# Performance work log

Measured on AMD Instinct MI355X. Metric: run time of the kernel, lower is better.

Reference implementation:

```python
import jax, jax.numpy as jnp
import numpy as np

B, S, QD, KVD, H = 8, 1024, 1024, 1024, 8
NEG_SLOPE = 0.01


def _lin(t, w, b):
    # torch nn.Linear: y = x @ W^T + b, W is (out, in)
    return t @ w.T + b


def _heads(t, n_head):
    b, s, e = t.shape
    return t.reshape(b, s, n_head, e // n_head).transpose(0, 2, 1, 3)  # (B,H,S,D)


def _merge(t):
    b, h, s, d = t.shape
    return t.transpose(0, 2, 1, 3).reshape(b, s, h * d)


def setup_inputs() -> dict:
    key = jax.random.key(0)
    ks = iter(jax.random.split(key, 64))

    def W(shape):
        return (jax.random.normal(next(ks), shape, jnp.float32) * 0.02)

    inp = {
        'x': jax.random.normal(next(ks), (B, S, QD), jnp.float32),
        'y': jax.random.normal(next(ks), (B, S, KVD), jnp.float32),
        # cross-attention projections
        'ca_q_w': W((QD, QD)), 'ca_q_b': W((QD,)),
        'ca_qv_w': W((QD, QD)), 'ca_qv_b': W((QD,)),
        'ca_k_w': W((QD, KVD)), 'ca_k_b': W((QD,)),
        'ca_kv_w': W((QD, KVD)), 'ca_kv_b': W((QD,)),
        'ca_o_w': W((QD, QD)), 'ca_o_b': W((QD,)),
        # LayerNorm over [seq_len, q_dim]
        'ln_w': jnp.ones((S, QD), jnp.float32),
        'ln_b': jnp.zeros((S, QD), jnp.float32),
        # 3-layer FeedForward
        'ff1_w': W((QD, QD)), 'ff1_b': W((QD,)),
        'ff2_w': W((QD, QD)), 'ff2_b': W((QD,)),
        'ff3_w': W((QD, QD)), 'ff3_b': W((QD,)),
        # self-attention 1
        'sa1_q_w': W((QD, QD)), 'sa1_q_b': W((QD,)),
        'sa1_k_w': W((QD, QD)), 'sa1_k_b': W((QD,)),
        'sa1_v_w': W((QD, QD)), 'sa1_v_b': W((QD,)),
        'sa1_o_w': W((QD, QD)), 'sa1_o_b': W((QD,)),
        # self-attention 2
        'sa2_q_w': W((QD, QD)), 'sa2_q_b': W((QD,)),
        'sa2_k_w': W((QD, QD)), 'sa2_k_b': W((QD,)),
        'sa2_v_w': W((QD, QD)), 'sa2_v_b': W((QD,)),
        'sa2_o_w': W((QD, QD)), 'sa2_o_b': W((QD,)),
    }
    return inp


def _self_attn(t, qw, qb, kw, kb, vw, vb, ow, ob):
    q = _heads(_lin(t, qw, qb), H)
    k = _heads(_lin(t, kw, kb), H)
    v = _heads(_lin(t, vw, vb), H)
    scale = 1.0 / jnp.sqrt(jnp.asarray(q.shape[-1], q.dtype))
    a = jax.nn.softmax(jnp.einsum('bhsd,bhtd->bhst', q, k) * scale, axis=-1)
    return _lin(_merge(jnp.einsum('bhst,bhtd->bhsd', a, v)), ow, ob)


def reference(x, y, ca_q_w, ca_q_b, ca_qv_w, ca_qv_b, ca_k_w, ca_k_b, ca_kv_w, ca_kv_b, ca_o_w, ca_o_b, ln_w, ln_b, ff1_w, ff1_b, ff2_w, ff2_b, ff3_w, ff3_b, sa1_q_w, sa1_q_b, sa1_k_w, sa1_k_b, sa1_v_w, sa1_v_b, sa1_o_w, sa1_o_b, sa2_q_w, sa2_q_b, sa2_k_w, sa2_k_b, sa2_v_w, sa2_v_b, sa2_o_w, sa2_o_b):
    # --- FlowFace cross-attention (no 1/sqrt(d) scaling, +QV term) ---
    q = _heads(_lin(x, ca_q_w, ca_q_b), H)
    qv = _heads(_lin(x, ca_qv_w, ca_qv_b), H)
    k = _heads(_lin(y, ca_k_w, ca_k_b), H)
    kv = _heads(_lin(y, ca_kv_w, ca_kv_b), H)
    attn = jax.nn.softmax(jnp.einsum('bhsd,bhtd->bhst', q, k), axis=-1)
    ca = _lin(_merge(jnp.einsum('bhst,bhtd->bhsd', attn, kv) + qv), ca_o_w, ca_o_b)
    h1 = x + ca
    # --- LayerNorm over last two dims [seq_len, q_dim] ---
    mu = h1.mean(axis=(-2, -1), keepdims=True)
    var = h1.var(axis=(-2, -1), keepdims=True)
    hn = (h1 - mu) / jnp.sqrt(var + 1e-5) * ln_w + ln_b
    # --- 3-layer FeedForward with leaky_relu + residual ---
    lr = lambda t: jax.nn.leaky_relu(t, NEG_SLOPE)
    f = lr(_lin(lr(_lin(lr(_lin(hn, ff1_w, ff1_b)), ff2_w, ff2_b)), ff3_w, ff3_b))
    h2 = hn + f
    # --- two self-attention layers ---
    h3 = _self_attn(h2, sa1_q_w, sa1_q_b, sa1_k_w, sa1_k_b, sa1_v_w, sa1_v_b, sa1_o_w, sa1_o_b)
    out = _self_attn(h3, sa2_q_w, sa2_q_b, sa2_k_w, sa2_k_b, sa2_v_w, sa2_v_b, sa2_o_w, sa2_o_b)
    return out
```

## Files before the change

kernel.cpp:

```cpp
#include <hip/hip_runtime.h>
#include <cstdint>
#include <cstddef>

#define DI __device__ __forceinline__

typedef __bf16 bf16x8 __attribute__((ext_vector_type(8)));
typedef float  f32x4  __attribute__((ext_vector_type(4)));

constexpr int kE = 1024;
constexpr int kM = 8192;
constexpr float kSlope = 0.01f;

DI float bf2f(ushort u) { union { uint32_t i; float f; } v; v.i = ((uint32_t)u) << 16; return v.f; }
DI ushort f2bf(float f) {
    union { float f; uint32_t i; } v; v.f = f;
    return (ushort)((v.i + 0x7FFFu + ((v.i >> 16) & 1u)) >> 16);
}
DI bf16x8 ld8f(const float* p) {
    const float4 f0 = *(const float4*)p;
    const float4 f1 = *(const float4*)(p + 4);
    union { bf16x8 v; ushort u[8]; } o;
    o.u[0] = f2bf(f0.x); o.u[1] = f2bf(f0.y); o.u[2] = f2bf(f0.z); o.u[3] = f2bf(f0.w);
    o.u[4] = f2bf(f1.x); o.u[5] = f2bf(f1.y); o.u[6] = f2bf(f1.z); o.u[7] = f2bf(f1.w);
    return o.v;
}
template<typename T> DI float ldf(const T* p);
template<> DI float ldf<ushort>(const ushort* p) { return bf2f(*p); }
template<> DI float ldf<float>(const float* p) { return *p; }

DI void gload16(const void* g, void* lds) {
    __builtin_amdgcn_global_load_lds((const __attribute__((address_space(1))) void*)g,
                                     (__attribute__((address_space(3))) void*)lds, 16, 0, 0);
}

DI int swz7(int r) { return ((r ^ (r >> 3)) & 7) << 4; }

struct PtrTab { const float* w[16]; const float* b[16]; const float* x; const float* y; };

__global__ __launch_bounds__(256)
void cvt_pack(PtrTab t, ushort* __restrict__ WB, ushort* __restrict__ Xb,
              ushort* __restrict__ Yb, float* __restrict__ BP)
{
    const int blk = blockIdx.x, tid = threadIdx.x;
    if (blk < 16384) {
        const float* src; ushort* dst; size_t idx;
        if (blk < 8192)       { const int w = blk >> 9; idx = (size_t)(blk & 511) * 2048 + tid * 8; src = t.w[w]; dst = WB + (size_t)w * 1048576; }
        else if (blk < 12288) { idx = (size_t)(blk - 8192) * 2048 + tid * 8;  src = t.x; dst = Xb; }
        else                  { idx = (size_t)(blk - 12288) * 2048 + tid * 8; src = t.y; dst = Yb; }
        *(bf16x8*)(dst + idx) = ld8f(src + idx);
    } else {
        const size_t i = (size_t)(blk - 16384) * 2048 + tid * 8;
        const int w = (int)(i >> 10), off = (int)(i & 1023);
        *(float4*)(BP + i)     = *(const float4*)(t.b[w] + off);
        *(float4*)(BP + i + 4) = *(const float4*)(t.b[w] + off + 4);
    }
}

template<int ACT, int RESID, typename TR, typename TO>
__global__ __launch_bounds__(256)
void gemm_bf16(const ushort* __restrict__ A, const ushort* __restrict__ W,
               const float* __restrict__ bias, const TR* __restrict__ resb,
               TO* __restrict__ out, int N)
{
    __shared__ __align__(16) char sm[2][16384];
    constexpr int K = 1024;
    const int tid = threadIdx.x, l = tid & 63, wid = tid >> 6;
    const int wm = wid >> 1, wn = wid & 1;

    const int cpx = gridDim.x >> 3;
    const int sb = (blockIdx.x & 7) * cpx + (blockIdx.x >> 3);
    const int nbn = N >> 7;
    const int bm = sb / nbn, bn = sb - bm * nbn;
    const size_t row0 = (size_t)bm << 7, col0 = (size_t)bn << 7;

    const int o0 = (wid * 2) * 1024 + (l << 4), o1 = o0 + 1024;
    const int r0s = o0 >> 6, c0s = ((o0 >> 4) & 3) ^ ((r0s >> 1) & 3);
    const int r1s = o1 >> 6, c1s = ((o1 >> 4) & 3) ^ ((r1s >> 1) & 3);
    const ushort* gA0 = A + (row0 + r0s) * K + c0s * 8;
    const ushort* gA1 = A + (row0 + r1s) * K + c1s * 8;
    const ushort* gW0 = W + (col0 + r0s) * K + c0s * 8;
    const ushort* gW1 = W + (col0 + r1s) * K + c1s * 8;
    const int d0 = (wid * 2) * 1024, d1 = d0 + 1024;

    f32x4 acc[4][4] = {};

    {
        gload16(gA0, sm[0] + d0); gload16(gA1, sm[0] + d1);
        gload16(gW0, sm[0] + 8192 + d0); gload16(gW1, sm[0] + 8192 + d1);
    }
    __syncthreads();

    for (int kt = 0; kt < 32; ++kt) {
        const int cur = kt & 1;
        if (kt + 1 < 32) {
            const int ko = (kt + 1) << 5;
            char* nb = sm[cur ^ 1];
            gload16(gA0 + ko, nb + d0); gload16(gA1 + ko, nb + d1);
            gload16(gW0 + ko, nb + 8192 + d0); gload16(gW1 + ko, nb + 8192 + d1);
        }
        const char* At = sm[cur];
        const char* Wt = sm[cur] + 8192;
        bf16x8 af[4], bfr[4];
        #pragma unroll
        for (int mi = 0; mi < 4; ++mi) {
            const int r = (wm << 6) + (mi << 4) + (l & 15);
            af[mi] = *(const bf16x8*)(At + r * 64 + ((((l >> 4) ^ ((r >> 1) & 3))) << 4));
        }
        #pragma unroll
        for (int ni = 0; ni < 4; ++ni) {
            const int r = (wn << 6) + (ni << 4) + (l & 15);
            bfr[ni] = *(const bf16x8*)(Wt + r * 64 + ((((l >> 4) ^ ((r >> 1) & 3))) << 4));
        }
        #pragma unroll
        for (int mi = 0; mi < 4; ++mi)
            #pragma unroll
            for (int ni = 0; ni < 4; ++ni)
                acc[mi][ni] = __builtin_amdgcn_mfma_f32_16x16x32_bf16(af[mi], bfr[ni], acc[mi][ni], 0, 0, 0);
        __syncthreads();
    }

    const int cr = (l >> 4) << 2, cc = l & 15;
    #pragma unroll
    for (int mi = 0; mi < 4; ++mi) {
        #pragma unroll
        for (int ni = 0; ni < 4; ++ni) {
            const size_t gr = row0 + (wm << 6) + (mi << 4) + cr;
            const size_t gc = col0 + (wn << 6) + (ni << 4) + cc;
            const float bv = bias[gc];
            #pragma unroll
            for (int r = 0; r < 4; ++r) {
                float v = acc[mi][ni][r] + bv;
                if (ACT) v = v > 0.f ? v : v * kSlope;
                const size_t off = (gr + r) * (size_t)N + gc;
                if (RESID) v += ldf(resb + off);
                if constexpr (sizeof(TO) == 4) out[off] = v;
                else                           out[off] = f2bf(v);
            }
        }
    }
}

template<int ADD_QV>
__global__ __launch_bounds__(256)
void attn_fwd(const ushort* __restrict__ Q, const ushort* __restrict__ K,
              const ushort* __restrict__ V, const ushort* __restrict__ QV,
              ushort* __restrict__ O, int ld, float scale)
{
    __shared__ __align__(16) char Kt[64 * 256];
    __shared__ __align__(16) char Vt[128 * 128];
    __shared__ __align__(16) char Pl[4][2048];

    const int tid = threadIdx.x;
    const int l = tid & 63, w = tid >> 6;

    const int cpx = gridDim.x >> 3;
    const int sb = (blockIdx.x & 7) * cpx + (blockIdx.x >> 3);
    const int qt = sb & 15;
    const int bh = sb >> 4;
    const int h = bh & 7, b = bh >> 3;

    const size_t bi = ((size_t)b << 10) * (size_t)ld + ((size_t)h << 7);
    const size_t bo = ((size_t)b << 10) * 1024 + ((size_t)h << 7);
    const size_t qrow0 = (size_t)(qt << 6) + (w << 4);

    bf16x8 qf[4];
    #pragma unroll
    for (int kk = 0; kk < 4; ++kk)
        qf[kk] = *(const bf16x8*)(Q + bi + (qrow0 + (l & 15)) * ld + (kk << 5) + ((l >> 4) << 3));

    f32x4 oacc[8] = {};
    float mrow[4] = {-1e30f, -1e30f, -1e30f, -1e30f};
    float lrow[4] = {0.f, 0.f, 0.f, 0.f};

    const int sr = tid >> 4, sc = tid & 15;

    for (int kt0 = 0; kt0 < 16; ++kt0) {
        __syncthreads();
        #pragma unroll
        for (int it = 0; it < 4; ++it) {
            const int r = sr + (it << 4);
            const size_t grow = bi + (size_t)(kt0 * 64 + r) * ld + (sc << 3);
            uint4 kv = *(const uint4*)(K + grow);
            *(uint4*)(Kt + r * 256 + ((sc << 4) ^ swz7(r))) = kv;
            uint4 vv = *(const uint4*)(V + grow);
            const ushort* e = (const ushort*)&vv;
            #pragma unroll
            for (int j = 0; j < 8; ++j) {
                const int d = (sc << 3) + j;
                *(ushort*)(Vt + d * 128 + ((r * 2) ^ swz7(d))) = e[j];
            }
        }
        __syncthreads();

        f32x4 sacc[4] = {};
        #pragma unroll
        for (int ni = 0; ni < 4; ++ni) {
            const int r = (l & 15) + (ni << 4);
            #pragma unroll
            for (int kk = 0; kk < 4; ++kk) {
                bf16x8 kf = *(const bf16x8*)(Kt + r * 256 + ((((kk << 2) + (l >> 4)) << 4) ^ swz7(r)));
                sacc[ni] = __builtin_amdgcn_mfma_f32_16x16x32_bf16(qf[kk], kf, sacc[ni], 0, 0, 0);
            }
        }
        #pragma unroll
        for (int ni = 0; ni < 4; ++ni) sacc[ni] *= scale;

        float corr[4];
        #pragma unroll
        for (int r = 0; r < 4; ++r) {
            float m0 = fmaxf(fmaxf(sacc[0][r], sacc[1][r]), fmaxf(sacc[2][r], sacc[3][r]));
            #pragma unroll
            for (int m = 1; m < 16; m <<= 1) m0 = fmaxf(m0, __shfl_xor(m0, m, 64));
            const float mn = fmaxf(mrow[r], m0);
            corr[r] = __expf(mrow[r] - mn);
            mrow[r] = mn;
        }
        float ps[4] = {0.f, 0.f, 0.f, 0.f};
        ushort pb[4][4];
        #pragma unroll
        for (int ni = 0; ni < 4; ++ni)
            #pragma unroll
            for (int r = 0; r < 4; ++r) {
                const float p = __expf(sacc[ni][r] - mrow[r]);
                ps[r] += p;
                pb[ni][r] = f2bf(p);
            }
        #pragma unroll
        for (int r = 0; r < 4; ++r) {
            float s = ps[r];
            #pragma unroll
            for (int m = 1; m < 16; m <<= 1) s += __shfl_xor(s, m, 64);
            lrow[r] = lrow[r] * corr[r] + s;
        }
        #pragma unroll
        for (int nd = 0; nd < 8; ++nd)
            #pragma unroll
            for (int r = 0; r < 4; ++r) oacc[nd][r] *= corr[r];

        char* pw = Pl[w];
        #pragma unroll
        for (int ni = 0; ni < 4; ++ni)
            #pragma unroll
            for (int r = 0; r < 4; ++r) {
                const int q = ((l >> 4) << 2) + r;
                const int t = (l & 15) + (ni << 4);
                *(ushort*)(pw + q * 128 + ((t * 2) ^ swz7(q))) = pb[ni][r];
            }
        #pragma unroll
        for (int tg = 0; tg < 2; ++tg) {
            const int q = l & 15;
            bf16x8 pf = *(const bf16x8*)(pw + q * 128 + ((((tg << 2) + (l >> 4)) << 4) ^ swz7(q)));
            #pragma unroll
            for (int nd = 0; nd < 8; ++nd) {
                const int d = (l & 15) + (nd << 4);
                bf16x8 vf = *(const bf16x8*)(Vt + d * 128 + ((((tg << 2) + (l >> 4)) << 4) ^ swz7(d)));
                oacc[nd] = __builtin_amdgcn_mfma_f32_16x16x32_bf16(pf, vf, oacc[nd], 0, 0, 0);
            }
        }
    }

    const size_t orow = qrow0 + ((l >> 4) << 2);
    #pragma unroll
    for (int r = 0; r < 4; ++r) {
        const float inv = 1.f / lrow[r];
        #pragma unroll
        for (int nd = 0; nd < 8; ++nd) {
            const size_t c = (l & 15) + (nd << 4);
            float v = oacc[nd][r] * inv;
            if (ADD_QV) v += bf2f(QV[bi + (orow + r) * ld + c]);
            O[bo + (orow + r) * 1024 + c] = f2bf(v);
        }
    }
}

__global__ void ln_partial(const ushort* __restrict__ h1, float2* __restrict__ part)
{
    __shared__ float sa[8];
    const size_t off = ((size_t)blockIdx.x) << 15;
    float s = 0.f, s2 = 0.f;
    for (int i = threadIdx.x; i < 4096; i += 256) {
        uint4 u = *(const uint4*)(h1 + off + (size_t)i * 8);
        const ushort* e = (const ushort*)&u;
        #pragma unroll
        for (int j = 0; j < 8; ++j) { const float v = bf2f(e[j]); s += v; s2 += v * v; }
    }
    #pragma unroll
    for (int m = 1; m < 64; m <<= 1) { s += __shfl_xor(s, m, 64); s2 += __shfl_xor(s2, m, 64); }
    const int w = threadIdx.x >> 6;
    if ((threadIdx.x & 63) == 0) { sa[w * 2] = s; sa[w * 2 + 1] = s2; }
    __syncthreads();
    if (threadIdx.x == 0)
        part[blockIdx.x] = make_float2(sa[0] + sa[2] + sa[4] + sa[6], sa[1] + sa[3] + sa[5] + sa[7]);
}

__global__ void ln_finish(const float2* __restrict__ part, float2* __restrict__ stats)
{
    const int b = threadIdx.x;
    if (b < 8) {
        float s = 0.f, s2 = 0.f;
        for (int c = 0; c < 32; ++c) { const float2 v = part[b * 32 + c]; s += v.x; s2 += v.y; }
        const float mu = s * (1.f / 1048576.f);
        const float var = s2 * (1.f / 1048576.f) - mu * mu;
        stats[b] = make_float2(mu, rsqrtf(var + 1e-5f));
    }
}

__global__ void ln_apply(const ushort* __restrict__ h1, const float2* __restrict__ stats,
                         const float* __restrict__ gw, const float* __restrict__ gb,
                         ushort* __restrict__ hn)
{
    const size_t i = ((size_t)blockIdx.x * 256 + threadIdx.x) * 8;
    const int b = (int)(i >> 20);
    const size_t r = i & 1048575;
    const float2 st = stats[b];
    uint4 uv = *(const uint4*)(h1 + i);
    const float4 w0 = *(const float4*)(gw + r);
    const float4 w1 = *(const float4*)(gw + r + 4);
    const float4 b0 = *(const float4*)(gb + r);
    const float4 b1 = *(const float4*)(gb + r + 4);
    const float wv[8] = {w0.x, w0.y, w0.z, w0.w, w1.x, w1.y, w1.z, w1.w};
    const float bv[8] = {b0.x, b0.y, b0.z, b0.w, b1.x, b1.y, b1.z, b1.w};
    const ushort* ev = (const ushort*)&uv;
    ushort o[8];
    #pragma unroll
    for (int j = 0; j < 8; ++j)
        o[j] = f2bf((bf2f(ev[j]) - st.x) * st.y * wv[j] + bv[j]);
    *(uint4*)(hn + i) = *(const uint4*)o;
}

extern "C" void kernel_launch(void* const* d_in, const int* in_sizes, int n_in,
                              void* d_out, int out_size, void* d_ws, size_t ws_size,
                              hipStream_t stream)
{
    (void)in_sizes; (void)n_in; (void)out_size; (void)ws_size;
    auto P = [&](int i) { return (const float*)d_in[i]; };

    const size_t MB = 1u << 20;
    char* ws = (char*)d_ws;
    ushort* WB = (ushort*)ws;
    ushort* R0 = (ushort*)(ws + 32 * MB);
    ushort* R1 = (ushort*)(ws + 64 * MB);
    ushort* A0 = (ushort*)(ws + 96 * MB);
    ushort* A1 = (ushort*)(ws + 112 * MB);
    float*  BP = (float*)(ws + 128 * MB);
    float2* PART = (float2*)(ws + 128 * MB + 65536);
    float2* STATS = PART + 256;

    PtrTab tab;
    const int wsrc[16] = {2,4,6,8,10,14,16,18,20,22,24,26,28,30,32,34};
    for (int i = 0; i < 16; ++i) { tab.w[i] = P(wsrc[i]); tab.b[i] = P(wsrc[i] + 1); }
    tab.x = P(0); tab.y = P(1);

    const dim3 blk(256);
    const float SA_SCALE = 0.08838834764831845f;
    auto Wp = [&](int w) { return WB + (size_t)w * 1048576; };
    auto Bp = [&](int w) { return BP + (size_t)w * 1024; };

    cvt_pack<<<dim3(16392), blk, 0, stream>>>(tab, WB, A0, A1, BP);

    gemm_bf16<0,0,ushort,ushort><<<dim3(1024), blk, 0, stream>>>(A0, Wp(0), Bp(0), (const ushort*)nullptr, R0, 2048);
    gemm_bf16<0,0,ushort,ushort><<<dim3(1024), blk, 0, stream>>>(A1, Wp(2), Bp(2), (const ushort*)nullptr, R1, 2048);
    attn_fwd<1><<<dim3(1024), blk, 0, stream>>>(R0, R1, R1 + 1024, R0 + 1024, A0, 2048, 1.0f);
    gemm_bf16<0,1,float,ushort><<<dim3(512), blk, 0, stream>>>(A0, Wp(4), Bp(4), P(0), A1, 1024);

    ln_partial<<<dim3(256), blk, 0, stream>>>(A1, PART);
    ln_finish<<<dim3(1), dim3(64), 0, stream>>>(PART, STATS);
    ln_apply<<<dim3(4096), blk, 0, stream>>>(A1, STATS, P(12), P(13), A0);

    gemm_bf16<1,0,ushort,ushort><<<dim3(512), blk, 0, stream>>>(A0, Wp(5), Bp(5), (const ushort*)nullptr, R0, 1024);
    gemm_bf16<1,0,ushort,ushort><<<dim3(512), blk, 0, stream>>>(R0, Wp(6), Bp(6), (const ushort*)nullptr, R1, 1024);
    gemm_bf16<1,1,ushort,ushort><<<dim3(512), blk, 0, stream>>>(R1, Wp(7), Bp(7), A0, A1, 1024);

    gemm_bf16<0,0,ushort,ushort><<<dim3(1536), blk, 0, stream>>>(A1, Wp(8), Bp(8), (const ushort*)nullptr, R0, 3072);
    attn_fwd<0><<<dim3(1024), blk, 0, stream>>>(R0, R0 + 1024, R0 + 2048, nullptr, A0, 3072, SA_SCALE);
    gemm_bf16<0,0,ushort,ushort><<<dim3(512), blk, 0, stream>>>(A0, Wp(11), Bp(11), (const ushort*)nullptr, A1, 1024);

    gemm_bf16<0,0,ushort,ushort><<<dim3(1536), blk, 0, stream>>>(A1, Wp(12), Bp(12), (const ushort*)nullptr, R0, 3072);
    attn_fwd<0><<<dim3(1024), blk, 0, stream>>>(R0, R0 + 1024, R0 + 2048, nullptr, A0, 3072, SA_SCALE);
    gemm_bf16<0,0,ushort,float><<<dim3(512), blk, 0, stream>>>(A0, Wp(15), Bp(15), (const ushort*)nullptr, (float*)d_out, 1024);
}
```

Measured before the change: 798.8 us.

## Emit V transposed from projection GEMM epilogue to avoid scalar LDS transpose in attention

For the V-producing column blocks, the projection GEMM swaps its MFMA operands so each lane holds a transposed tile, then writes V directly in a per-head [d][t] layout. The attention kernel then loads V with 16-byte vector copies into a swizzled LDS tile instead of scattering eight 2-byte stores per element. This removes the costly scalar LDS transpose in every attention key tile. In exchange, the GEMM epilogue does strided 2-byte global stores for V, and the buffer assignments in the launch sequence are reshuffled.

Result: slower. 876.3 us (+9.7%).

```diff
diff --git a/kernel.cpp b/kernel.cpp
--- a/kernel.cpp
+++ b/kernel.cpp
@@ -56,11 +56,11 @@
     }
 }
 
-template<int ACT, int RESID, typename TR, typename TO>
+template<int ACT, int RESID, int VT, typename TR, typename TO>
 __global__ __launch_bounds__(256)
 void gemm_bf16(const ushort* __restrict__ A, const ushort* __restrict__ W,
                const float* __restrict__ bias, const TR* __restrict__ resb,
-               TO* __restrict__ out, int N)
+               TO* __restrict__ out, int N, ushort* __restrict__ vt_out, int vtcol0)
 {
     __shared__ __align__(16) char sm[2][16384];
     constexpr int K = 1024;
@@ -72,6 +72,7 @@
     const int nbn = N >> 7;
     const int bm = sb / nbn, bn = sb - bm * nbn;
     const size_t row0 = (size_t)bm << 7, col0 = (size_t)bn << 7;
+    const bool isvt = VT && ((int)col0 >= vtcol0);
 
     const int o0 = (wid * 2) * 1024 + (l << 4), o1 = o0 + 1024;
     const int r0s = o0 >> 6, c0s = ((o0 >> 4) & 3) ^ ((r0s >> 1) & 3);
@@ -111,30 +112,57 @@
             const int r = (wn << 6) + (ni << 4) + (l & 15);
             bfr[ni] = *(const bf16x8*)(Wt + r * 64 + ((((l >> 4) ^ ((r >> 1) & 3))) << 4));
         }
-        #pragma unroll
-        for (int mi = 0; mi < 4; ++mi)
-            #pragma unroll
-            for (int ni = 0; ni < 4; ++ni)
-                acc[mi][ni] = __builtin_amdgcn_mfma_f32_16x16x32_bf16(af[mi], bfr[ni], acc[mi][ni], 0, 0, 0);
+        if (!isvt) {
+            #pragma unroll
+            for (int mi = 0; mi < 4; ++mi)
+                #pragma unroll
+                for (int ni = 0; ni < 4; ++ni)
+                    acc[mi][ni] = __builtin_amdgcn_mfma_f32_16x16x32_bf16(af[mi], bfr[ni], acc[mi][ni], 0, 0, 0);
+        } else {
+            #pragma unroll
+            for (int mi = 0; mi < 4; ++mi)
+                #pragma unroll
+                for (int ni = 0; ni < 4; ++ni)
+                    acc[mi][ni] = __builtin_amdgcn_mfma_f32_16x16x32_bf16(bfr[ni], af[mi], acc[mi][ni], 0, 0, 0);
+        }
         __syncthreads();
     }
 
     const int cr = (l >> 4) << 2, cc = l & 15;
-    #pragma unroll
-    for (int mi = 0; mi < 4; ++mi) {
-        #pragma unroll
-        for (int ni = 0; ni < 4; ++ni) {
-            const size_t gr = row0 + (wm << 6) + (mi << 4) + cr;
-            const size_t gc = col0 + (wn << 6) + (ni << 4) + cc;
-            const float bv = bias[gc];
-            #pragma unroll
-            for (int r = 0; r < 4; ++r) {
-                float v = acc[mi][ni][r] + bv;
-                if (ACT) v = v > 0.f ? v : v * kSlope;
-                const size_t off = (gr + r) * (size_t)N + gc;
-                if (RESID) v += ldf(resb + off);
-                if constexpr (sizeof(TO) == 4) out[off] = v;
-                else                           out[off] = f2bf(v);
+    if (!isvt) {
+        #pragma unroll
+        for (int mi = 0; mi < 4; ++mi) {
+            #pragma unroll
+            for (int ni = 0; ni < 4; ++ni) {
+                const size_t gr = row0 + (wm << 6) + (mi << 4) + cr;
+                const size_t gc = col0 + (wn << 6) + (ni << 4) + cc;
+                const float bv = bias[gc];
+                #pragma unroll
+                for (int r = 0; r < 4; ++r) {
+                    float v = acc[mi][ni][r] + bv;
+                    if (ACT) v = v > 0.f ? v : v * kSlope;
+                    const size_t off = (gr + r) * (size_t)N + gc;
+                    if (RESID) v += ldf(resb + off);
+                    if constexpr (sizeof(TO) == 4) out[off] = v;
+                    else                           out[off] = f2bf(v);
+                }
+            }
+        }
+    } else if (VT) {
+        #pragma unroll
+        for (int mi = 0; mi < 4; ++mi) {
+            const size_t t_glob = row0 + (wm << 6) + (mi << 4) + cc;
+            const size_t bb = t_glob >> 10;
+            const int tt = (int)(t_glob & 1023);
+            #pragma unroll
+            for (int ni = 0; ni < 4; ++ni) {
+                const int gcb = (int)col0 + (wn << 6) + (ni << 4) + cr;
+                const int dbase = gcb - vtcol0;
+                #pragma unroll
+                for (int r = 0; r < 4; ++r) {
+                    const float v = acc[mi][ni][r] + bias[gcb + r];
+                    vt_out[(((bb << 10) + dbase + r) << 10) + tt] = f2bf(v);
+                }
             }
         }
     }
@@ -143,7 +171,7 @@
 template<int ADD_QV>
 __global__ __launch_bounds__(256)
 void attn_fwd(const ushort* __restrict__ Q, const ushort* __restrict__ K,
-              const ushort* __restrict__ V, const ushort* __restrict__ QV,
+              const ushort* __restrict__ VT, const ushort* __restrict__ QV,
               ushort* __restrict__ O, int ld, float scale)
 {
     __shared__ __align__(16) char Kt[64 * 256];
@@ -161,6 +189,7 @@
 
     const size_t bi = ((size_t)b << 10) * (size_t)ld + ((size_t)h << 7);
     const size_t bo = ((size_t)b << 10) * 1024 + ((size_t)h << 7);
+    const size_t vtoff = ((size_t)bh) << 17;
     const size_t qrow0 = (size_t)(qt << 6) + (w << 4);
 
     bf16x8 qf[4];
@@ -174,21 +203,28 @@
 
     const int sr = tid >> 4, sc = tid & 15;
 
+    int vofs[4];
+    #pragma unroll
+    for (int it = 0; it < 4; ++it) {
+        const int d = it * 32 + (tid >> 3);
+        const int s = tid & 7;
+        const int c = s ^ ((d ^ (d >> 3)) & 7);
+        vofs[it] = d * 1024 + c * 8;
+    }
+    const int vdst = tid * 16;
+
     for (int kt0 = 0; kt0 < 16; ++kt0) {
         __syncthreads();
         #pragma unroll
         for (int it = 0; it < 4; ++it) {
             const int r = sr + (it << 4);
-            const size_t grow = bi + (size_t)(kt0 * 64 + r) * ld + (sc << 3);
-            uint4 kv = *(const uint4*)(K + grow);
+            uint4 kv = *(const uint4*)(K + bi + (size_t)(kt0 * 64 + r) * ld + (sc << 3));
             *(uint4*)(Kt + r * 256 + ((sc << 4) ^ swz7(r))) = kv;
-            uint4 vv = *(const uint4*)(V + grow);
-            const ushort* e = (const ushort*)&vv;
-            #pragma unroll
-            for (int j = 0; j < 8; ++j) {
-                const int d = (sc << 3) + j;
-                *(ushort*)(Vt + d * 128 + ((r * 2) ^ swz7(d))) = e[j];
-            }
+        }
+        #pragma unroll
+        for (int it = 0; it < 4; ++it) {
+            uint4 vv = *(const uint4*)(VT + vtoff + (size_t)(kt0 << 6) + vofs[it]);
+            *(uint4*)(Vt + it * 4096 + vdst) = vv;
         }
         __syncthreads();
 
@@ -252,8 +288,9 @@
             bf16x8 pf = *(const bf16x8*)(pw + q * 128 + ((((tg << 2) + (l >> 4)) << 4) ^ swz7(q)));
             #pragma unroll
             for (int nd = 0; nd < 8; ++nd) {
-                const int d = (l & 15) + (nd << 4);
-                bf16x8 vf = *(const bf16x8*)(Vt + d * 128 + ((((tg << 2) + (l >> 4)) << 4) ^ swz7(d)));
+                const int d = (nd << 4) + (l & 15);
+                const int m = (d ^ (d >> 3)) & 7;
+                bf16x8 vf = *(const bf16x8*)(Vt + d * 128 + ((((tg << 2) + (l >> 4)) ^ m) << 4));
                 oacc[nd] = __builtin_amdgcn_mfma_f32_16x16x32_bf16(pf, vf, oacc[nd], 0, 0, 0);
             }
         }
@@ -358,24 +395,24 @@
 
     cvt_pack<<<dim3(16392), blk, 0, stream>>>(tab, WB, A0, A1, BP);
 
-    gemm_bf16<0,0,ushort,ushort><<<dim3(1024), blk, 0, stream>>>(A0, Wp(0), Bp(0), (const ushort*)nullptr, R0, 2048);
-    gemm_bf16<0,0,ushort,ushort><<<dim3(1024), blk, 0, stream>>>(A1, Wp(2), Bp(2), (const ushort*)nullptr, R1, 2048);
-    attn_fwd<1><<<dim3(1024), blk, 0, stream>>>(R0, R1, R1 + 1024, R0 + 1024, A0, 2048, 1.0f);
-    gemm_bf16<0,1,float,ushort><<<dim3(512), blk, 0, stream>>>(A0, Wp(4), Bp(4), P(0), A1, 1024);
-
-    ln_partial<<<dim3(256), blk, 0, stream>>>(A1, PART);
+    gemm_bf16<0,0,0,ushort,ushort><<<dim3(1024), blk, 0, stream>>>(A0, Wp(0), Bp(0), (const ushort*)nullptr, R0, 2048, nullptr, 0);
+    gemm_bf16<0,0,1,ushort,ushort><<<dim3(1024), blk, 0, stream>>>(A1, Wp(2), Bp(2), (const ushort*)nullptr, R1, 2048, A0, 1024);
+    attn_fwd<1><<<dim3(1024), blk, 0, stream>>>(R0, R1, A0, R0 + 1024, A1, 2048, 1.0f);
+    gemm_bf16<0,1,0,float,ushort><<<dim3(512), blk, 0, stream>>>(A1, Wp(4), Bp(4), P(0), A0, 1024, nullptr, 0);
+
+    ln_partial<<<dim3(256), blk, 0, stream>>>(A0, PART);
     ln_finish<<<dim3(1), dim3(64), 0, stream>>>(PART, STATS);
-    ln_apply<<<dim3(4096), blk, 0, stream>>>(A1, STATS, P(12), P(13), A0);
-
-    gemm_bf16<1,0,ushort,ushort><<<dim3(512), blk, 0, stream>>>(A0, Wp(5), Bp(5), (const ushort*)nullptr, R0, 1024);
-    gemm_bf16<1,0,ushort,ushort><<<dim3(512), blk, 0, stream>>>(R0, Wp(6), Bp(6), (const ushort*)nullptr, R1, 1024);
-    gemm_bf16<1,1,ushort,ushort><<<dim3(512), blk, 0, stream>>>(R1, Wp(7), Bp(7), A0, A1, 1024);
-
-    gemm_bf16<0,0,ushort,ushort><<<dim3(1536), blk, 0, stream>>>(A1, Wp(8), Bp(8), (const ushort*)nullptr, R0, 3072);
-    attn_fwd<0><<<dim3(1024), blk, 0, stream>>>(R0, R0 + 1024, R0 + 2048, nullptr, A0, 3072, SA_SCALE);
-    gemm_bf16<0,0,ushort,ushort><<<dim3(512), blk, 0, stream>>>(A0, Wp(11), Bp(11), (const ushort*)nullptr, A1, 1024);
-
-    gemm_bf16<0,0,ushort,ushort><<<dim3(1536), blk, 0, stream>>>(A1, Wp(12), Bp(12), (const ushort*)nullptr, R0, 3072);
-    attn_fwd<0><<<dim3(1024), blk, 0, stream>>>(R0, R0 + 1024, R0 + 2048, nullptr, A0, 3072, SA_SCALE);
-    gemm_bf16<0,0,ushort,float><<<dim3(512), blk, 0, stream>>>(A0, Wp(15), Bp(15), (const ushort*)nullptr, (float*)d_out, 1024);
-}
+    ln_apply<<<dim3(4096), blk, 0, stream>>>(A0, STATS, P(12), P(13), A1);
+
+    gemm_bf16<1,0,0,ushort,ushort><<<dim3(512), blk, 0, stream>>>(A1, Wp(5), Bp(5), (const ushort*)nullptr, R0, 1024, nullptr, 0);
+    gemm_bf16<1,0,0,ushort,ushort><<<dim3(512), blk, 0, stream>>>(R0, Wp(6), Bp(6), (const ushort*)nullptr, R1, 1024, nullptr, 0);
+    gemm_bf16<1,1,0,ushort,ushort><<<dim3(512), blk, 0, stream>>>(R1, Wp(7), Bp(7), A1, A0, 1024, nullptr, 0);
+
+    gemm_bf16<0,0,1,ushort,ushort><<<dim3(1536), blk, 0, stream>>>(A0, Wp(8), Bp(8), (const ushort*)nullptr, R0, 3072, A1, 2048);
+    attn_fwd<0><<<dim3(1024), blk, 0, stream>>>(R0, R0 + 1024, A1, nullptr, A0, 3072, SA_SCALE);
+    gemm_bf16<0,0,0,ushort,ushort><<<dim3(512), blk, 0, stream>>>(A0, Wp(11), Bp(11), (const ushort*)nullptr, A1, 1024, nullptr, 0);
+
+    gemm_bf16<0,0,1,ushort,ushort><<<dim3(1536), blk, 0, stream>>>(A1, Wp(12), Bp(12), (const ushort*)nullptr, R0, 3072, A0, 2048);
+    attn_fwd<0><<<dim3(1024), blk, 0, stream>>>(R0, R0 + 1024, A0, nullptr, A1, 3072, SA_SCALE);
+    gemm_bf16<0,0,0,ushort,float><<<dim3(512), blk, 0, stream>>>(A1, Wp(15), Bp(15), (const ushort*)nullptr, (float*)d_out, 1024, nullptr, 0);
+}
```
